# Optimization experiments

Hardware: AMD Instinct MI355X
Metric: run time of the kernel (lower is better)

## Reference

```python
import jax, jax.numpy as jnp
import numpy as np
from jax import lax

# --- static config (mirrors cfg / init args) ---
B, T, F_IN = 4, 1024, 80      # batch, time steps, mel bins (80 -> freq collapses to 1)
C_EMB = 512                   # cfg.dim_embed
C0 = C_EMB // 2               # first_conv_filters (non-tcn branch)
HEADS, K = 8, 7               # num_heads, NA kernel_size (dilation=1)
D_HEAD = C_EMB // HEADS
MLP = 4 * C_EMB               # mlp_ratio=4
EPS = 1e-5                    # layer_norm_eps


def setup_inputs() -> dict:
    key = jax.random.key(0)
    ks = jax.random.split(key, 16)
    rn = lambda k, s, sc=0.02: jax.random.normal(k, s, dtype=jnp.float32) * sc
    z = lambda *s: jnp.zeros(s, dtype=jnp.float32)
    o = lambda *s: jnp.ones(s, dtype=jnp.float32)
    return {
        "x": jax.random.normal(ks[0], (B, 1, T, F_IN), dtype=jnp.float32),
        # conv embedding stack (OIHW)
        "conv0_w": rn(ks[1], (C0, 1, 3, 3), 0.1), "conv0_b": z(C0),
        "conv1_w": rn(ks[2], (C_EMB, C0, 1, 12), 0.02), "conv1_b": z(C_EMB),
        "conv2_w": rn(ks[3], (C_EMB, C_EMB, 3, 3), 0.02), "conv2_b": z(C_EMB),
        "emb_ln_g": o(C_EMB), "emb_ln_b": z(C_EMB),
        # neighborhood attention (linear weights stored [in,out]; apply as x @ W + b)
        "q_w": rn(ks[4], (C_EMB, C_EMB)), "q_b": z(C_EMB),
        "k_w": rn(ks[5], (C_EMB, C_EMB)), "k_b": z(C_EMB),
        "v_w": rn(ks[6], (C_EMB, C_EMB)), "v_b": z(C_EMB),
        "rpb": rn(ks[7], (HEADS, 2 * K - 1)),
        "attn_out_w": rn(ks[8], (C_EMB, C_EMB)), "attn_out_b": z(C_EMB),
        "ln1_g": o(C_EMB), "ln1_b": z(C_EMB),
        "ln2_g": o(C_EMB), "ln2_b": z(C_EMB),
        "mlp1_w": rn(ks[9], (C_EMB, MLP)), "mlp1_b": z(MLP),
        "mlp2_w": rn(ks[10], (MLP, C_EMB)), "mlp2_b": z(C_EMB),
    }


def _layer_norm(x, g, b):
    m = jnp.mean(x, axis=-1, keepdims=True)
    v = jnp.mean(jnp.square(x - m), axis=-1, keepdims=True)
    return (x - m) * lax.rsqrt(v + EPS) * g + b


def _na1d(q, k, v, rpb):
    """1D neighborhood attention (natten1dqkrpb + softmax + natten1dav), dilation=1.
    q,k,v: [B,H,T,D]; rpb: [H,2K-1]. Returns [B,H,T,D]."""
    Bq, H, Tq, D = q.shape
    ni = jnp.clip(jnp.arange(Tq) - K // 2, 0, Tq - K)        # window start per query
    idx = ni[:, None] + jnp.arange(K)                         # [T,K] key positions
    k_win = k[:, :, idx]                                      # [B,H,T,K,D]
    v_win = v[:, :, idx]                                      # [B,H,T,K,D]
    scores = jnp.einsum('bhtd,bhtkd->bhtk', q, k_win)
    rel = idx - jnp.arange(Tq)[:, None] + (K - 1)             # [T,K] in [0,2K-2]
    scores = scores + rpb[:, rel][None]                       # + [1,H,T,K]
    probs = jax.nn.softmax(scores, axis=-1)
    return jnp.einsum('bhtk,bhtkd->bhtd', probs, v_win)


def _forward(x, conv0_w, conv0_b, conv1_w, conv1_b, conv2_w, conv2_b,
             emb_ln_g, emb_ln_b, q_w, q_b, k_w, k_b, v_w, v_b, rpb,
             attn_out_w, attn_out_b, ln1_g, ln1_b, ln2_g, ln2_b,
             mlp1_w, mlp1_b, mlp2_w, mlp2_b):
    conv = lambda h, w, b, pad: lax.conv_general_dilated(
        h, w, (1, 1), pad, dimension_numbers=('NCHW', 'OIHW', 'NCHW')
    ) + b[None, :, None, None]
    pool3 = lambda h: lax.reduce_window(h, -jnp.inf, lax.max,
                                        (1, 1, 1, 3), (1, 1, 1, 3), 'VALID')
    # --- AllInOneEmbeddings (eval: dropouts are no-ops) ---
    h = jax.nn.relu(pool3(conv(x, conv0_w, conv0_b, [(1, 1), (0, 0)])))
    h = jax.nn.relu(pool3(conv(h, conv1_w, conv1_b, [(0, 0), (0, 0)])))
    h = jax.nn.relu(pool3(conv(h, conv2_w, conv2_b, [(1, 1), (0, 0)])))
    h = jnp.transpose(h[..., 0], (0, 2, 1))                   # [B,T,C]
    emb = _layer_norm(h, emb_ln_g, emb_ln_b)
    # --- DinatLayer1d (double_attention=False, drop_path=0) ---
    Bh, Th, Ch = emb.shape
    shortcut = emb
    hs = _layer_norm(emb, ln1_g, ln1_b)
    heads = lambda y: jnp.transpose(y.reshape(Bh, Th, HEADS, D_HEAD), (0, 2, 1, 3))
    q = heads(hs @ q_w + q_b) * (1.0 / jnp.sqrt(jnp.float32(D_HEAD)))
    kk = heads(hs @ k_w + k_b)
    vv = heads(hs @ v_w + v_b)
    ctx = _na1d(q, kk, vv, rpb)                               # [B,H,T,D]
    ctx = jnp.transpose(ctx, (0, 2, 1, 3)).reshape(Bh, Th, Ch)
    attn = ctx @ attn_out_w + attn_out_b                      # NeighborhoodAttentionOutput
    hs = shortcut + attn
    ln = _layer_norm(hs, ln2_g, ln2_b)
    mlp = jax.nn.gelu(ln @ mlp1_w + mlp1_b, approximate=False) @ mlp2_w + mlp2_b
    return hs + mlp


def reference(x, conv0_w, conv0_b, conv1_w, conv1_b, conv2_w, conv2_b,
              emb_ln_g, emb_ln_b, q_w, q_b, k_w, k_b, v_w, v_b, rpb,
              attn_out_w, attn_out_b, ln1_g, ln1_b, ln2_g, ln2_b,
              mlp1_w, mlp1_b, mlp2_w, mlp2_b):
    return _forward(x, conv0_w, conv0_b, conv1_w, conv1_b, conv2_w, conv2_b,
                    emb_ln_g, emb_ln_b, q_w, q_b, k_w, k_b, v_w, v_b, rpb,
                    attn_out_w, attn_out_b, ln1_g, ln1_b, ln2_g, ln2_b,
                    mlp1_w, mlp1_b, mlp2_w, mlp2_b)
```

## Files before the change

kernel.cpp:

```cpp
#include <hip/hip_runtime.h>
#include <hip/hip_bf16.h>
#include <math.h>


typedef __bf16 bf16x8 __attribute__((ext_vector_type(8)));
typedef float f32x4 __attribute__((ext_vector_type(4)));

static __device__ __forceinline__ short f2bf(float f) {
  __hip_bfloat16 h = __float2bfloat16(f);
  return __builtin_bit_cast(short, h);
}

static __device__ __forceinline__ float wave_sum(float v) {
#pragma unroll
  for (int o = 32; o; o >>= 1) v += __shfl_xor(v, o);
  return v;
}

static __device__ __forceinline__ void gld16(const void* g, void* l) {
  __builtin_amdgcn_global_load_lds(
      (const __attribute__((address_space(1))) unsigned int*)g,
      (__attribute__((address_space(3))) unsigned int*)l, 16, 0, 0);
}

__global__ __launch_bounds__(256) void conv0_kernel(
    const float* __restrict__ x, const float* __restrict__ w,
    const float* __restrict__ bias, short* __restrict__ h0) {
  const int b = blockIdx.x >> 10;
  const int t = blockIdx.x & 1023;
  const int c = threadIdx.x;
  __shared__ float xs[3][80];
  for (int i = threadIdx.x; i < 240; i += 256) {
    int dt = i / 80, f = i - dt * 80;
    int tt = t + dt - 1;
    xs[dt][f] = (tt >= 0 && tt < 1024) ? x[(b * 1024 + tt) * 80 + f] : 0.f;
  }
  float wr[9];
#pragma unroll
  for (int i = 0; i < 9; ++i) wr[i] = w[c * 9 + i];
  const float bi = bias[c];
  __syncthreads();
  const int cc = c >> 5, q = (c >> 3) & 3, e = c & 7;
  short* outb = &h0[((size_t)(b * 8 + cc) * 1024 + t) * 832];
  for (int fo = 0; fo < 26; ++fo) {
    float m = -1e30f;
#pragma unroll
    for (int p = 0; p < 3; ++p) {
      const int f = fo * 3 + p;
      float acc = bi;
#pragma unroll
      for (int dt = 0; dt < 3; ++dt)
#pragma unroll
        for (int df = 0; df < 3; ++df)
          acc += xs[dt][f + df] * wr[dt * 3 + df];
      m = fmaxf(m, acc);
    }
    const int row = t * 26 + fo;
    outb[fo * 32 + (q ^ ((row >> 1) & 3)) * 8 + e] = f2bf(fmaxf(m, 0.f));
  }
}

__global__ __launch_bounds__(256) void prep_w1(const float* __restrict__ w,
                                               short* __restrict__ wt) {
  const int co = blockIdx.x;
  __shared__ float ls[3072];
  for (int i = threadIdx.x; i < 3072; i += 256) ls[i] = w[co * 3072 + i];
  __syncthreads();
  const int swz = (co >> 1) & 3;
  for (int i = threadIdx.x; i < 3072; i += 256) {
    const int e = i & 7, q = (i >> 3) & 3, kw = (i >> 5) % 12, cc = i / 384;
    const int ci = cc * 32 + q * 8 + e;
    wt[(((size_t)(cc * 12 + kw) * 512 + co) * 4 + (q ^ swz)) * 8 + e] =
        f2bf(ls[ci * 12 + kw]);
  }
}

__global__ __launch_bounds__(256) void prep_w2(const float* __restrict__ w,
                                               short* __restrict__ wt) {
  const int co = blockIdx.x;
  __shared__ float ls[4608];
  for (int i = threadIdx.x; i < 4608; i += 256) ls[i] = w[co * 4608 + i];
  __syncthreads();
  const int swz = (co >> 1) & 3;
  for (int i = threadIdx.x; i < 4608; i += 256) {
    const int e = i & 7, q = (i >> 3) & 3, p = (i >> 5) % 9, cc = i / 288;
    const int ci = cc * 32 + q * 8 + e;
    wt[(((size_t)(cc * 9 + p) * 512 + co) * 4 + (q ^ swz)) * 8 + e] =
        f2bf(ls[ci * 9 + p]);
  }
}

__global__ void prep_wt(const float* __restrict__ w, short* __restrict__ wt,
                        int K, int N) {
  __shared__ float tile[32][33];
  const int k0 = blockIdx.x * 32, n0 = blockIdx.y * 32;
  const int tx = threadIdx.x, ty = threadIdx.y;
  for (int r = ty; r < 32; r += 8) tile[r][tx] = w[(size_t)(k0 + r) * N + n0 + tx];
  __syncthreads();
  for (int r = ty; r < 32; r += 8) wt[(size_t)(n0 + r) * K + k0 + tx] = f2bf(tile[tx][r]);
}

__global__ __launch_bounds__(256) void zero_h1_edges(short* __restrict__ h1) {
  short* base = h1 + (size_t)blockIdx.x * 164160;
  for (int i = threadIdx.x; i < 160; i += 256) {
    base[i] = 0;
    base[1025 * 160 + i] = 0;
  }
}

__global__ __launch_bounds__(512) void conv1_kernel(
    const short* __restrict__ h0, const short* __restrict__ wt1,
    const float* __restrict__ bias, short* __restrict__ h1) {
  const int b = blockIdx.x >> 5;
  const int t0 = (blockIdx.x & 31) * 32;
  const int co0 = blockIdx.y * 128;
  __shared__ short XsF[2][26688];
  __shared__ short AsF[2][12288];
  const int tid = threadIdx.x;
  const int lane = tid & 63;
  const int wid = tid >> 6;
  const int wm = wid >> 2;
  const int wn = wid & 3;
  const int l15 = lane & 15, lg = lane >> 4;

  const f32x4 zf = {0.f, 0.f, 0.f, 0.f};
  f32x4 acc[4][8];
#pragma unroll
  for (int i = 0; i < 4; ++i)
#pragma unroll
    for (int j = 0; j < 8; ++j) acc[i][j] = zf;

  auto stageX = [&](int cc, int buf) {
    const short* xs = h0 + ((size_t)(b * 8 + cc) * 1024 + t0) * 832;
#pragma unroll
    for (int i = 0; i < 7; ++i) {
      const int v = wid + 8 * i;
      if (v < 52) gld16(xs + v * 512 + lane * 8, &XsF[buf][v * 512]);
    }
  };
  auto stageA = [&](int cc, int g, int buf) {
#pragma unroll
    for (int i = 0; i < 3; ++i) {
      const int u = wid * 3 + i;
      const int kwl = u >> 3, r = u & 7;
      gld16(wt1 + ((size_t)((cc * 12 + g * 3 + kwl) * 512) + co0) * 32 +
                r * 512 + lane * 8,
            &AsF[buf][kwl * 4096 + r * 512]);
    }
  };

  stageX(0, 0);
  stageA(0, 0, 0);
  __syncthreads();

  for (int s = 0; s < 32; ++s) {
    const int cc = s >> 2, g = s & 3;
    if (s < 31) {
      const int s1 = s + 1;
      const int cc1 = s1 >> 2, g1 = s1 & 3;
      stageA(cc1, g1, s1 & 1);
      if (g1 == 0) stageX(cc1, cc1 & 1);
    }
    const short* Xb = XsF[cc & 1];
    const short* Ab = AsF[s & 1];
#pragma unroll
    for (int j = 0; j < 3; ++j) {
      const int kw = g * 3 + j;
      bf16x8 a[4];
#pragma unroll
      for (int sm = 0; sm < 4; ++sm) {
        const int co_l = wm * 64 + sm * 16 + l15;
        a[sm] = *reinterpret_cast<const bf16x8*>(
            &Ab[(j * 512 + co_l * 4 + (lg ^ ((co_l >> 1) & 3))) * 8]);
      }
#pragma unroll
      for (int sn = 0; sn < 8; ++sn) {
        const int row = (wn * 8 + sn) * 26 + l15 + kw;
        bf16x8 bf = *reinterpret_cast<const bf16x8*>(
            &Xb[(row * 4 + (lg ^ ((row >> 1) & 3))) * 8]);
#pragma unroll
        for (int sm = 0; sm < 4; ++sm)
          acc[sm][sn] = __builtin_amdgcn_mfma_f32_16x16x32_bf16(a[sm], bf, acc[sm][sn], 0, 0, 0);
      }
    }
    __syncthreads();
  }
  const int basel = lane & 48;
  const int wsrc = (l15 < 5) ? 3 * l15 : 0;
#pragma unroll
  for (int sm = 0; sm < 4; ++sm)
#pragma unroll
    for (int sn = 0; sn < 8; ++sn) {
      const int t = t0 + wn * 8 + sn;
#pragma unroll
      for (int r = 0; r < 4; ++r) {
        float val = acc[sm][sn][r];
        float v0 = __shfl(val, basel + wsrc);
        float v1 = __shfl(val, basel + wsrc + 1);
        float v2 = __shfl(val, basel + wsrc + 2);
        if (l15 < 5) {
          const int co = co0 + wm * 64 + sm * 16 + lg * 4 + r;
          float p = fmaxf(fmaxf(v0, v1), v2) + bias[co];
          const int cc2 = co >> 5, q = (co >> 3) & 3, e = co & 7;
          const int row_g = (t + 1) * 5 + l15;
          h1[((size_t)(b * 16 + cc2) * 1026 + (t + 1)) * 160 + l15 * 32 +
             (q ^ ((row_g >> 1) & 3)) * 8 + e] = f2bf(fmaxf(p, 0.f));
        }
      }
    }
}

__global__ __launch_bounds__(512) void conv2_kernel(
    const short* __restrict__ h1, const short* __restrict__ wt2,
    const float* __restrict__ bias, float* __restrict__ emb_in) {
  const int b = blockIdx.x >> 5;
  const int t0 = (blockIdx.x & 31) * 32;
  const int co0 = blockIdx.y * 128;
  __shared__ __align__(16) short smem2[35840];
  const int tid = threadIdx.x;
  const int lane = tid & 63;
  const int wid = tid >> 6;
  const int wm = wid >> 1;
  const int wn = wid & 1;
  const int l15 = lane & 15, lg = lane >> 4;
  const f32x4 zf = {0.f, 0.f, 0.f, 0.f};
  f32x4 acc[2][3];
#pragma unroll
  for (int i = 0; i < 2; ++i)
#pragma unroll
    for (int j = 0; j < 3; ++j) acc[i][j] = zf;
  int tl[3], dwl[3];
#pragma unroll
  for (int sn = 0; sn < 3; ++sn) {
    const int c = wn * 48 + sn * 16 + l15;
    tl[sn] = c / 3;
    dwl[sn] = c - tl[sn] * 3;
  }

  auto stageX = [&](int cc, int buf) {
    const short* xs = h1 + ((size_t)(b * 16 + cc) * 1026 + t0) * 160;
#pragma unroll
    for (int i = 0; i < 2; ++i) {
      const int v = wid + 8 * i;
      if (v < 11) gld16(xs + v * 512 + lane * 8, &smem2[buf * 5632 + v * 512]);
    }
  };
  auto stageA = [&](int cc, int g, int buf) {
#pragma unroll
    for (int i = 0; i < 3; ++i) {
      const int u = wid * 3 + i;
      const int pl = u >> 3, r = u & 7;
      gld16(wt2 + ((size_t)((cc * 9 + g * 3 + pl) * 512) + co0) * 32 +
                r * 512 + lane * 8,
            &smem2[11264 + buf * 12288 + pl * 4096 + r * 512]);
    }
  };

  stageX(0, 0);
  stageA(0, 0, 0);
  __syncthreads();

  for (int s = 0; s < 48; ++s) {
    const int cc = s / 3, g = s - cc * 3;
    if (s < 47) {
      const int s1 = s + 1;
      const int cc1 = s1 / 3, g1 = s1 - cc1 * 3;
      stageA(cc1, g1, s1 & 1);
      if (g1 == 0) stageX(cc1, cc1 & 1);
    }
    const short* Xb = &smem2[(cc & 1) * 5632];
    const short* Ab = &smem2[11264 + (s & 1) * 12288];
#pragma unroll
    for (int j = 0; j < 3; ++j) {
      bf16x8 a[2];
#pragma unroll
      for (int sm = 0; sm < 2; ++sm) {
        const int co_l = wm * 32 + sm * 16 + l15;
        a[sm] = *reinterpret_cast<const bf16x8*>(
            &Ab[(j * 512 + co_l * 4 + (lg ^ ((co_l >> 1) & 3))) * 8]);
      }
#pragma unroll
      for (int sn = 0; sn < 3; ++sn) {
        const int row = (tl[sn] + g) * 5 + dwl[sn] + j;
        bf16x8 xv = *reinterpret_cast<const bf16x8*>(
            &Xb[(row * 4 + (lg ^ ((row >> 1) & 3))) * 8]);
#pragma unroll
        for (int sm = 0; sm < 2; ++sm)
          acc[sm][sn] = __builtin_amdgcn_mfma_f32_16x16x32_bf16(a[sm], xv, acc[sm][sn], 0, 0, 0);
      }
    }
    __syncthreads();
  }
  float(*Ds)[100] = reinterpret_cast<float(*)[100]>(smem2);
#pragma unroll
  for (int sm = 0; sm < 2; ++sm)
#pragma unroll
    for (int sn = 0; sn < 3; ++sn)
#pragma unroll
      for (int r = 0; r < 4; ++r)
        Ds[wm * 32 + sm * 16 + lg * 4 + r][wn * 48 + sn * 16 + l15] = acc[sm][sn][r];
  __syncthreads();
  for (int e = tid; e < 4096; e += 512) {
    const int co = e & 127, tt = e >> 7;
    float m = fmaxf(fmaxf(Ds[co][tt * 3], Ds[co][tt * 3 + 1]), Ds[co][tt * 3 + 2]) + bias[co0 + co];
    emb_in[((size_t)(b * 1024) + t0 + tt) * 512 + co0 + co] = fmaxf(m, 0.f);
  }
}

__global__ __launch_bounds__(256) void ln_double_kernel(
    const float* __restrict__ x, const float* __restrict__ g0,
    const float* __restrict__ b0, const float* __restrict__ g1,
    const float* __restrict__ b1, float* __restrict__ o0, float* __restrict__ o1) {
  const int row = blockIdx.x * 4 + (threadIdx.x >> 6);
  const int lane = threadIdx.x & 63;
  const float* xr = x + (size_t)row * 512;
  float v[8];
#pragma unroll
  for (int j = 0; j < 8; ++j) v[j] = xr[j * 64 + lane];
  float s = 0;
#pragma unroll
  for (int j = 0; j < 8; ++j) s += v[j];
  s = wave_sum(s);
  const float mean = s * (1.f / 512.f);
  float q = 0;
#pragma unroll
  for (int j = 0; j < 8; ++j) { float d = v[j] - mean; q += d * d; }
  q = wave_sum(q);
  const float rs = rsqrtf(q * (1.f / 512.f) + 1e-5f);
#pragma unroll
  for (int j = 0; j < 8; ++j) {
    const int ci = j * 64 + lane;
    float e = (v[j] - mean) * rs * g0[ci] + b0[ci];
    o0[(size_t)row * 512 + ci] = e;
    v[j] = e;
  }
  s = 0;
#pragma unroll
  for (int j = 0; j < 8; ++j) s += v[j];
  s = wave_sum(s);
  const float mean2 = s * (1.f / 512.f);
  q = 0;
#pragma unroll
  for (int j = 0; j < 8; ++j) { float d = v[j] - mean2; q += d * d; }
  q = wave_sum(q);
  const float rs2 = rsqrtf(q * (1.f / 512.f) + 1e-5f);
#pragma unroll
  for (int j = 0; j < 8; ++j) {
    const int ci = j * 64 + lane;
    o1[(size_t)row * 512 + ci] = (v[j] - mean2) * rs2 * g1[ci] + b1[ci];
  }
}

__global__ __launch_bounds__(256) void ln_kernel(
    const float* __restrict__ x, const float* __restrict__ g,
    const float* __restrict__ b, float* __restrict__ o) {
  const int row = blockIdx.x * 4 + (threadIdx.x >> 6);
  const int lane = threadIdx.x & 63;
  const float* xr = x + (size_t)row * 512;
  float v[8];
#pragma unroll
  for (int j = 0; j < 8; ++j) v[j] = xr[j * 64 + lane];
  float s = 0;
#pragma unroll
  for (int j = 0; j < 8; ++j) s += v[j];
  s = wave_sum(s);
  const float mean = s * (1.f / 512.f);
  float q = 0;
#pragma unroll
  for (int j = 0; j < 8; ++j) { float d = v[j] - mean; q += d * d; }
  q = wave_sum(q);
  const float rs = rsqrtf(q * (1.f / 512.f) + 1e-5f);
#pragma unroll
  for (int j = 0; j < 8; ++j) {
    const int ci = j * 64 + lane;
    o[(size_t)row * 512 + ci] = (v[j] - mean) * rs * g[ci] + b[ci];
  }
}

__global__ __launch_bounds__(256) void na1d_kernel(
    const float* __restrict__ q, const float* __restrict__ k,
    const float* __restrict__ v, const float* __restrict__ rpb,
    float* __restrict__ ctx) {
  const int W = blockIdx.x * 4 + (threadIdx.x >> 6);
  const int lane = threadIdx.x & 63;
  const int b = W >> 13, h = (W >> 10) & 7, t = W & 1023;
  int ni = t - 3;
  ni = ni < 0 ? 0 : (ni > 1017 ? 1017 : ni);
  const size_t base = (size_t)(b * 1024) * 512 + h * 64;
  const float qv = q[base + (size_t)t * 512 + lane];
  const float* kb = k + base + (size_t)ni * 512;
  float s[7];
#pragma unroll
  for (int j = 0; j < 7; ++j) {
    float pd = qv * kb[j * 512 + lane];
    pd = wave_sum(pd);
    s[j] = pd + rpb[h * 13 + (ni + j - t + 6)];
  }
  float mx = s[0];
#pragma unroll
  for (int j = 1; j < 7; ++j) mx = fmaxf(mx, s[j]);
  float den = 0;
#pragma unroll
  for (int j = 0; j < 7; ++j) { s[j] = expf(s[j] - mx); den += s[j]; }
  const float inv = 1.f / den;
  const float* vb = v + base + (size_t)ni * 512;
  float o = 0;
#pragma unroll
  for (int j = 0; j < 7; ++j) o += s[j] * vb[j * 512 + lane];
  ctx[base + (size_t)t * 512 + lane] = o * inv;
}

template <int EPI>
__global__ __launch_bounds__(256) void gemm_tf(
    const float* __restrict__ A, const short* __restrict__ Wt,
    const float* __restrict__ bias, const float* __restrict__ res,
    float* __restrict__ C, int K, int N) {
  const int m0 = blockIdx.x * 128, n0 = blockIdx.y * 64;
  __shared__ short Asm[128][40];
  __shared__ short Bsm[64][40];
  const int tid = threadIdx.x;
  const int wid = tid >> 6, lane = tid & 63;
  const int wm = wid >> 1, wn = wid & 1;
  const int l15 = lane & 15, lg = lane >> 4;
  const f32x4 zf = {0.f, 0.f, 0.f, 0.f};
  f32x4 acc[4][2];
#pragma unroll
  for (int i = 0; i < 4; ++i) { acc[i][0] = zf; acc[i][1] = zf; }
  const int ar = tid >> 1, ahf = (tid & 1) * 16;
  for (int k0 = 0; k0 < K; k0 += 32) {
    __syncthreads();
    {
      const float4* s = reinterpret_cast<const float4*>(&A[(size_t)(m0 + ar) * K + k0 + ahf]);
      float4 f0 = s[0], f1 = s[1], f2 = s[2], f3 = s[3];
      short* d = &Asm[ar][ahf];
      d[0] = f2bf(f0.x);  d[1] = f2bf(f0.y);  d[2] = f2bf(f0.z);  d[3] = f2bf(f0.w);
      d[4] = f2bf(f1.x);  d[5] = f2bf(f1.y);  d[6] = f2bf(f1.z);  d[7] = f2bf(f1.w);
      d[8] = f2bf(f2.x);  d[9] = f2bf(f2.y);  d[10] = f2bf(f2.z); d[11] = f2bf(f2.w);
      d[12] = f2bf(f3.x); d[13] = f2bf(f3.y); d[14] = f2bf(f3.z); d[15] = f2bf(f3.w);
    }
    if (tid < 128) {
      const int br = tid >> 1, bhf = (tid & 1) * 16;
      const int4* s = reinterpret_cast<const int4*>(&Wt[(size_t)(n0 + br) * K + k0 + bhf]);
      int4* d = reinterpret_cast<int4*>(&Bsm[br][bhf]);
      d[0] = s[0];
      d[1] = s[1];
    }
    __syncthreads();
    bf16x8 bfr[2];
#pragma unroll
    for (int sn = 0; sn < 2; ++sn)
      bfr[sn] = *reinterpret_cast<const bf16x8*>(&Bsm[wn * 32 + sn * 16 + l15][lg * 8]);
#pragma unroll
    for (int sm = 0; sm < 4; ++sm) {
      bf16x8 a = *reinterpret_cast<const bf16x8*>(&Asm[wm * 64 + sm * 16 + l15][lg * 8]);
#pragma unroll
      for (int sn = 0; sn < 2; ++sn)
        acc[sm][sn] = __builtin_amdgcn_mfma_f32_16x16x32_bf16(a, bfr[sn], acc[sm][sn], 0, 0, 0);
    }
  }
#pragma unroll
  for (int sm = 0; sm < 4; ++sm)
#pragma unroll
    for (int sn = 0; sn < 2; ++sn)
#pragma unroll
      for (int r = 0; r < 4; ++r) {
        const int m = m0 + wm * 64 + sm * 16 + lg * 4 + r;
        const int n = n0 + wn * 32 + sn * 16 + l15;
        float val = acc[sm][sn][r] + bias[n];
        if (EPI == 1) val *= 0.125f;
        if (EPI == 2) val = 0.5f * val * (1.f + erff(val * 0.70710678f));
        if (EPI == 3) val += res[(size_t)m * N + n];
        C[(size_t)m * N + n] = val;
      }
}

extern "C" void kernel_launch(void* const* d_in, const int* in_sizes, int n_in,
                              void* d_out, int out_size, void* d_ws, size_t ws_size,
                              hipStream_t stream) {
  (void)in_sizes; (void)n_in; (void)out_size;
  const float* x        = (const float*)d_in[0];
  const float* conv0_w  = (const float*)d_in[1];
  const float* conv0_b  = (const float*)d_in[2];
  const float* conv1_w  = (const float*)d_in[3];
  const float* conv1_b  = (const float*)d_in[4];
  const float* conv2_w  = (const float*)d_in[5];
  const float* conv2_b  = (const float*)d_in[6];
  const float* emb_ln_g = (const float*)d_in[7];
  const float* emb_ln_b = (const float*)d_in[8];
  const float* q_w  = (const float*)d_in[9];
  const float* q_b  = (const float*)d_in[10];
  const float* k_w  = (const float*)d_in[11];
  const float* k_b  = (const float*)d_in[12];
  const float* v_w  = (const float*)d_in[13];
  const float* v_b  = (const float*)d_in[14];
  const float* rpb  = (const float*)d_in[15];
  const float* ao_w = (const float*)d_in[16];
  const float* ao_b = (const float*)d_in[17];
  const float* ln1_g = (const float*)d_in[18];
  const float* ln1_b = (const float*)d_in[19];
  const float* ln2_g = (const float*)d_in[20];
  const float* ln2_b = (const float*)d_in[21];
  const float* m1_w = (const float*)d_in[22];
  const float* m1_b = (const float*)d_in[23];
  const float* m2_w = (const float*)d_in[24];
  const float* m2_b = (const float*)d_in[25];

  char* ws = (char*)d_ws;
  size_t off = 0;
  auto alloc = [&](size_t bytes) -> char* {
    char* p = ws + off;
    off += (bytes + 255) & ~(size_t)255;
    return p;
  };
  short* h0   = (short*)alloc(4ull * 8 * 1024 * 832 * 2);
  short* h1   = (short*)alloc(4ull * 16 * 1026 * 160 * 2);
  float* embi = (float*)alloc(4ull * 1024 * 512 * 4);
  float* emb  = (float*)alloc(4ull * 1024 * 512 * 4);
  float* hs1  = (float*)alloc(4ull * 1024 * 512 * 4);
  float* qb   = (float*)alloc(4ull * 1024 * 512 * 4);
  float* kb   = (float*)alloc(4ull * 1024 * 512 * 4);
  float* vb   = (float*)alloc(4ull * 1024 * 512 * 4);
  float* ctx  = (float*)alloc(4ull * 1024 * 512 * 4);
  float* hs   = (float*)alloc(4ull * 1024 * 512 * 4);
  short* wt1  = (short*)alloc(512ull * 12 * 256 * 2);
  short* wt2  = (short*)alloc(512ull * 9 * 512 * 2);
  short* wtq  = (short*)alloc(512ull * 512 * 2);
  short* wtk  = (short*)alloc(512ull * 512 * 2);
  short* wtv  = (short*)alloc(512ull * 512 * 2);
  short* wtao = (short*)alloc(512ull * 512 * 2);
  short* wtm1 = (short*)alloc(2048ull * 512 * 2);
  short* wtm2 = (short*)alloc(512ull * 2048 * 2);
  if (ws_size < off) return;
  float* mid  = (float*)h0;
  float* ln2o = embi;
  float* outp = (float*)d_out;

  prep_w1<<<512, 256, 0, stream>>>(conv1_w, wt1);
  prep_w2<<<512, 256, 0, stream>>>(conv2_w, wt2);
  zero_h1_edges<<<64, 256, 0, stream>>>(h1);
  dim3 tb(32, 8);
  prep_wt<<<dim3(16, 16), tb, 0, stream>>>(q_w, wtq, 512, 512);
  prep_wt<<<dim3(16, 16), tb, 0, stream>>>(k_w, wtk, 512, 512);
  prep_wt<<<dim3(16, 16), tb, 0, stream>>>(v_w, wtv, 512, 512);
  prep_wt<<<dim3(16, 16), tb, 0, stream>>>(ao_w, wtao, 512, 512);
  prep_wt<<<dim3(16, 64), tb, 0, stream>>>(m1_w, wtm1, 512, 2048);
  prep_wt<<<dim3(64, 16), tb, 0, stream>>>(m2_w, wtm2, 2048, 512);

  conv0_kernel<<<4096, 256, 0, stream>>>(x, conv0_w, conv0_b, h0);
  conv1_kernel<<<dim3(128, 4), 512, 0, stream>>>(h0, wt1, conv1_b, h1);
  conv2_kernel<<<dim3(128, 4), 512, 0, stream>>>(h1, wt2, conv2_b, embi);
  ln_double_kernel<<<1024, 256, 0, stream>>>(embi, emb_ln_g, emb_ln_b, ln1_g, ln1_b, emb, hs1);
  gemm_tf<1><<<dim3(32, 8), 256, 0, stream>>>(hs1, wtq, q_b, nullptr, qb, 512, 512);
  gemm_tf<0><<<dim3(32, 8), 256, 0, stream>>>(hs1, wtk, k_b, nullptr, kb, 512, 512);
  gemm_tf<0><<<dim3(32, 8), 256, 0, stream>>>(hs1, wtv, v_b, nullptr, vb, 512, 512);
  na1d_kernel<<<8192, 256, 0, stream>>>(qb, kb, vb, rpb, ctx);
  gemm_tf<3><<<dim3(32, 8), 256, 0, stream>>>(ctx, wtao, ao_b, emb, hs, 512, 512);
  ln_kernel<<<1024, 256, 0, stream>>>(hs, ln2_g, ln2_b, ln2o);
  gemm_tf<2><<<dim3(32, 32), 256, 0, stream>>>(ln2o, wtm1, m1_b, nullptr, mid, 512, 2048);
  gemm_tf<3><<<dim3(32, 8), 256, 0, stream>>>(mid, wtm2, m2_b, hs, outp, 2048, 512);
}
```

Baseline: 500.8 us.

## Pad conv0 rows, split conv1 K-steps finer, use explicit vmcnt waits

Pads the conv0 output rows from 26 to 28 frequency slots (stride 896), so each conv1 X tile stages as exactly 7 loads per wave with no bounds check. The padding is zero-filled. conv1 now processes 2 kernel widths per stage instead of 3, over 48 stages, which shrinks the A double buffer. Both conv1 and conv2 replace __syncthreads with explicit s_waitcnt vmcnt counts plus raw barriers, so the prefetch for the next stage can stay in flight while the current one computes. The hand-counted vmcnt values risk races if the compiler's load count differs, and the extra stages add more barriers.

```diff
diff --git a/kernel.cpp b/kernel.cpp
--- a/kernel.cpp
+++ b/kernel.cpp
@@ -41,7 +41,7 @@
   const float bi = bias[c];
   __syncthreads();
   const int cc = c >> 5, q = (c >> 3) & 3, e = c & 7;
-  short* outb = &h0[((size_t)(b * 8 + cc) * 1024 + t) * 832];
+  short* outb = &h0[((size_t)(b * 8 + cc) * 1024 + t) * 896];
   for (int fo = 0; fo < 26; ++fo) {
     float m = -1e30f;
 #pragma unroll
@@ -55,9 +55,10 @@
           acc += xs[dt][f + df] * wr[dt * 3 + df];
       m = fmaxf(m, acc);
     }
-    const int row = t * 26 + fo;
+    const int row = t * 28 + fo;
     outb[fo * 32 + (q ^ ((row >> 1) & 3)) * 8 + e] = f2bf(fmaxf(m, 0.f));
   }
+  if (c < 64) outb[832 + c] = 0;
 }
 
 __global__ __launch_bounds__(256) void prep_w1(const float* __restrict__ w,
@@ -114,8 +115,8 @@
   const int b = blockIdx.x >> 5;
   const int t0 = (blockIdx.x & 31) * 32;
   const int co0 = blockIdx.y * 128;
-  __shared__ short XsF[2][26688];
-  __shared__ short AsF[2][12288];
+  __shared__ short XsF[2][28672];
+  __shared__ short AsF[2][8192];
   const int tid = threadIdx.x;
   const int lane = tid & 63;
   const int wid = tid >> 6;
@@ -131,19 +132,19 @@
     for (int j = 0; j < 8; ++j) acc[i][j] = zf;
 
   auto stageX = [&](int cc, int buf) {
-    const short* xs = h0 + ((size_t)(b * 8 + cc) * 1024 + t0) * 832;
+    const short* xs = h0 + ((size_t)(b * 8 + cc) * 1024 + t0) * 896;
 #pragma unroll
     for (int i = 0; i < 7; ++i) {
-      const int v = wid + 8 * i;
-      if (v < 52) gld16(xs + v * 512 + lane * 8, &XsF[buf][v * 512]);
+      const int v = wid * 7 + i;
+      gld16(xs + v * 512 + lane * 8, &XsF[buf][v * 512]);
     }
   };
   auto stageA = [&](int cc, int g, int buf) {
 #pragma unroll
-    for (int i = 0; i < 3; ++i) {
-      const int u = wid * 3 + i;
+    for (int i = 0; i < 2; ++i) {
+      const int u = wid * 2 + i;
       const int kwl = u >> 3, r = u & 7;
-      gld16(wt1 + ((size_t)((cc * 12 + g * 3 + kwl) * 512) + co0) * 32 +
+      gld16(wt1 + ((size_t)((cc * 12 + g * 2 + kwl) * 512) + co0) * 32 +
                 r * 512 + lane * 8,
             &AsF[buf][kwl * 4096 + r * 512]);
     }
@@ -151,21 +152,30 @@
 
   stageX(0, 0);
   stageA(0, 0, 0);
-  __syncthreads();
-
-  for (int s = 0; s < 32; ++s) {
-    const int cc = s >> 2, g = s & 3;
-    if (s < 31) {
+  asm volatile("s_waitcnt vmcnt(0)" ::: "memory");
+  __builtin_amdgcn_s_barrier();
+
+  for (int s = 0; s < 48; ++s) {
+    const int cc = s / 6, g = s - cc * 6;
+    if (s < 47) {
       const int s1 = s + 1;
-      const int cc1 = s1 >> 2, g1 = s1 & 3;
+      const int cc1 = s1 / 6, g1 = s1 - cc1 * 6;
       stageA(cc1, g1, s1 & 1);
-      if (g1 == 0) stageX(cc1, cc1 & 1);
-    }
+      if (g1 == 0) {
+        stageX(cc1, cc1 & 1);
+        asm volatile("s_waitcnt vmcnt(9)" ::: "memory");
+      } else {
+        asm volatile("s_waitcnt vmcnt(2)" ::: "memory");
+      }
+    } else {
+      asm volatile("s_waitcnt vmcnt(0)" ::: "memory");
+    }
+    __builtin_amdgcn_s_barrier();
     const short* Xb = XsF[cc & 1];
     const short* Ab = AsF[s & 1];
 #pragma unroll
-    for (int j = 0; j < 3; ++j) {
-      const int kw = g * 3 + j;
+    for (int j = 0; j < 2; ++j) {
+      const int kw = g * 2 + j;
       bf16x8 a[4];
 #pragma unroll
       for (int sm = 0; sm < 4; ++sm) {
@@ -175,7 +185,7 @@
       }
 #pragma unroll
       for (int sn = 0; sn < 8; ++sn) {
-        const int row = (wn * 8 + sn) * 26 + l15 + kw;
+        const int row = (wn * 8 + sn) * 28 + l15 + kw;
         bf16x8 bf = *reinterpret_cast<const bf16x8*>(
             &Xb[(row * 4 + (lg ^ ((row >> 1) & 3))) * 8]);
 #pragma unroll
@@ -183,7 +193,8 @@
           acc[sm][sn] = __builtin_amdgcn_mfma_f32_16x16x32_bf16(a[sm], bf, acc[sm][sn], 0, 0, 0);
       }
     }
-    __syncthreads();
+    asm volatile("" ::: "memory");
+    __builtin_amdgcn_s_barrier();
   }
   const int basel = lane & 48;
   const int wsrc = (l15 < 5) ? 3 * l15 : 0;
@@ -258,7 +269,8 @@
 
   stageX(0, 0);
   stageA(0, 0, 0);
-  __syncthreads();
+  asm volatile("s_waitcnt vmcnt(0)" ::: "memory");
+  __builtin_amdgcn_s_barrier();
 
   for (int s = 0; s < 48; ++s) {
     const int cc = s / 3, g = s - cc * 3;
@@ -266,8 +278,17 @@
       const int s1 = s + 1;
       const int cc1 = s1 / 3, g1 = s1 - cc1 * 3;
       stageA(cc1, g1, s1 & 1);
-      if (g1 == 0) stageX(cc1, cc1 & 1);
-    }
+      if (g1 == 0) {
+        stageX(cc1, cc1 & 1);
+        if (wid < 3) asm volatile("s_waitcnt vmcnt(5)" ::: "memory");
+        else         asm volatile("s_waitcnt vmcnt(4)" ::: "memory");
+      } else {
+        asm volatile("s_waitcnt vmcnt(3)" ::: "memory");
+      }
+    } else {
+      asm volatile("s_waitcnt vmcnt(0)" ::: "memory");
+    }
+    __builtin_amdgcn_s_barrier();
     const short* Xb = &smem2[(cc & 1) * 5632];
     const short* Ab = &smem2[11264 + (s & 1) * 12288];
 #pragma unroll
@@ -289,7 +310,8 @@
           acc[sm][sn] = __builtin_amdgcn_mfma_f32_16x16x32_bf16(a[sm], xv, acc[sm][sn], 0, 0, 0);
       }
     }
-    __syncthreads();
+    asm volatile("" ::: "memory");
+    __builtin_amdgcn_s_barrier();
   }
   float(*Ds)[100] = reinterpret_cast<float(*)[100]>(smem2);
 #pragma unroll
@@ -512,7 +534,7 @@
     off += (bytes + 255) & ~(size_t)255;
     return p;
   };
-  short* h0   = (short*)alloc(4ull * 8 * 1024 * 832 * 2);
+  short* h0   = (short*)alloc(4ull * 8 * 1024 * 896 * 2);
   short* h1   = (short*)alloc(4ull * 16 * 1026 * 160 * 2);
   float* embi = (float*)alloc(4ull * 1024 * 512 * 4);
   float* emb  = (float*)alloc(4ull * 1024 * 512 * 4);
```

After: 499.5 us. Within noise of the previous version (-0.3%).
